# Optimization experiments

Measured on AMD Instinct MI355X. Metric: run time of the kernel, lower is better.

Reference implementation:

```python
import jax, jax.numpy as jnp
import numpy as np

N = 1000000   # total nodes
F = 32        # node feature dim
E = 8         # edge feature dim
K = 16        # kernels per degree
COUNTS = [200000, 300000, 300000, 200000]  # focal nodes per degree 1..4
EPS = 1e-8


def _cos_mat(a, b):
    # a: [n, f], b: [k, f] -> cosine sim [n, k]
    num = a @ b.T
    den = jnp.linalg.norm(a, axis=-1)[:, None] * jnp.linalg.norm(b, axis=-1)[None, :]
    return num / jnp.maximum(den, EPS)


def _cos_pairs(a, b):
    # a: [n, d, f], b: [k, d, f] -> mean over d of per-slot cosine sim -> [n, k]
    num = jnp.einsum('ndf,kdf->nkd', a, b)
    den = jnp.linalg.norm(a, axis=-1)[:, None, :] * jnp.linalg.norm(b, axis=-1)[None, :, :]
    return jnp.mean(num / jnp.maximum(den, EPS), axis=-1)


def _deg_score(x, sel, nei, nei_p, nei_e, Wc, Wn, Wp, We, d):
    nd = sel.shape[0]
    x_focal = x[sel]                     # [nd, F] degree-grouped gather
    x_nei = x[nei].reshape(nd, d, F)     # [nd, d, F]
    sc = (_cos_mat(x_focal, Wc) + _cos_pairs(x_nei, Wn)
          + _cos_pairs(nei_p, Wp) + _cos_pairs(nei_e, We)) * 0.25
    return sc                            # [nd, K]


def setup_inputs() -> dict:
    key = jax.random.key(0)
    ks = iter(jax.random.split(key, 64))
    perm = jax.random.permutation(next(ks), N)  # degree buckets partition all nodes
    inp = {"x": jax.random.normal(next(ks), (N, F), jnp.float32)}
    off = 0
    for d in range(1, 5):
        nd = COUNTS[d - 1]
        inp[f"sel{d}"] = perm[off:off + nd]
        off += nd
        inp[f"nei{d}"] = jax.random.randint(next(ks), (nd * d,), 0, N)
        inp[f"nei_p{d}"] = jax.random.normal(next(ks), (nd, d, 3), jnp.float32)
        inp[f"nei_e{d}"] = jax.random.uniform(next(ks), (nd, d, E), jnp.float32)
        inp[f"Wc{d}"] = jax.random.normal(next(ks), (K, F), jnp.float32)
        inp[f"Wn{d}"] = jax.random.normal(next(ks), (K, d, F), jnp.float32)
        inp[f"Wp{d}"] = jax.random.normal(next(ks), (K, d, 3), jnp.float32)
        inp[f"We{d}"] = jax.random.normal(next(ks), (K, d, E), jnp.float32)
    return inp


def reference(x,
              sel1, nei1, nei_p1, nei_e1, Wc1, Wn1, Wp1, We1,
              sel2, nei2, nei_p2, nei_e2, Wc2, Wn2, Wp2, We2,
              sel3, nei3, nei_p3, nei_e3, Wc3, Wn3, Wp3, We3,
              sel4, nei4, nei_p4, nei_e4, Wc4, Wn4, Wp4, We4):
    groups = [
        (sel1, nei1, nei_p1, nei_e1, Wc1, Wn1, Wp1, We1),
        (sel2, nei2, nei_p2, nei_e2, Wc2, Wn2, Wp2, We2),
        (sel3, nei3, nei_p3, nei_e3, Wc3, Wn3, Wp3, We3),
        (sel4, nei4, nei_p4, nei_e4, Wc4, Wn4, Wp4, We4),
    ]
    # equivalent to: fill [sum_K, N] block matrix grouped by degree, reorder
    # columns by argsort of concatenated selected indices, then transpose.
    out = jnp.zeros((N, 4 * K), x.dtype)
    for i, (sel, nei, npos, ne, wc, wn, wp, we) in enumerate(groups):
        sc = _deg_score(x, sel, nei, npos, ne, wc, wn, wp, we, i + 1)
        out = out.at[sel, i * K:(i + 1) * K].set(sc)
    return out
```

## Files before the change

kernel.cpp:

```cpp
#include <hip/hip_runtime.h>
#include <stdint.h>

typedef _Float16 half8 __attribute__((ext_vector_type(8)));
typedef float floatx4 __attribute__((ext_vector_type(4)));
typedef float fvec4 __attribute__((ext_vector_type(4)));

struct WPtrs { const float *wc, *wn, *wp, *we; };

struct PrepArgs {
  const float* x; _Float16* xhat; int N; int nb_norm;
  WPtrs w[4]; _Float16* psi;
};

__global__ __launch_bounds__(256) void k_prep(PrepArgs a) {
  int bid = blockIdx.x, tid = threadIdx.x;

  if (bid < a.nb_norm) {
    int row = bid * 64 + (tid >> 2);
    int q   = tid & 3;
    if (row >= a.N) return;
    const fvec4* xr = reinterpret_cast<const fvec4*>(a.x + (size_t)row * 32 + q * 8);
    fvec4 va = xr[0], vb = xr[1];
    float ss = va[0] * va[0] + va[1] * va[1] + va[2] * va[2] + va[3] * va[3] +
               vb[0] * vb[0] + vb[1] * vb[1] + vb[2] * vb[2] + vb[3] * vb[3];
    ss += __shfl_xor(ss, 1);
    ss += __shfl_xor(ss, 2);
    float rn = ss > 0.f ? rsqrtf(ss) : 0.f;
    half8 h;
    h[0] = (_Float16)(va[0] * rn); h[1] = (_Float16)(va[1] * rn);
    h[2] = (_Float16)(va[2] * rn); h[3] = (_Float16)(va[3] * rn);
    h[4] = (_Float16)(vb[0] * rn); h[5] = (_Float16)(vb[1] * rn);
    h[6] = (_Float16)(vb[2] * rn); h[7] = (_Float16)(vb[3] * rn);
    *reinterpret_cast<half8*>(a.xhat + (size_t)row * 32 + q * 8) = h;
    return;
  }

  int g = bid - a.nb_norm;
  int d = g + 1;
  int KD = 32 * (1 + d);
  _Float16* pg = a.psi + (size_t)g * (16 * 160);

  int k     = tid & 15;
  int piece = tid >> 4;
  if (piece > d) return;
  const float* src;
  float scale;
  if (piece == 0) { src = a.w[g].wc + k * 32;                           scale = 0.25f; }
  else            { src = a.w[g].wn + (size_t)(k * d + piece - 1) * 32; scale = 0.25f / d; }
  float ss = 0.f;
  for (int j = 0; j < 32; ++j) ss += src[j] * src[j];
  float n  = sqrtf(ss);
  float sc = n > 0.f ? scale / n : 0.f;
  _Float16* dst = pg + k * KD + 32 * piece;
  for (int j = 0; j < 32; ++j) dst[j] = (_Float16)(src[j] * sc);
}

struct MainArgs {
  const _Float16* xhat;
  const _Float16* psi;
  const int* sel[4];
  const int* nei[4];
  const float* p[4];
  const float* e[4];
  WPtrs w[4];
  float* out;
  int nd[4];
  int blkOff[5];
};

template <int D, int NCH>
__device__ inline void main_one(const MainArgs& a, int g, int blk) {
  constexpr int NF = 1 + D;
  constexpr int KD = 32 * NF;
  constexpr int NM = (D + 1) / 2;

  const _Float16* xhat = a.xhat;
  const _Float16* psi  = a.psi + (size_t)g * (16 * 160);
  const int* sel = a.sel[g];
  const int* nei = a.nei[g];
  const float* __restrict__ pptr = a.p[g];
  const float* __restrict__ eptr = a.e[g];
  int nd = a.nd[g];

  int wave    = threadIdx.x >> 6;
  int lane    = threadIdx.x & 63;
  int nchunks = (nd + 15) >> 4;
  int chunk0  = (blk * 4 + wave) * NCH;
  if (chunk0 >= nchunks) return;
  int r = lane & 15;
  int c = lane >> 4;

  half8 bx[NF];
  {
    const _Float16* pb = psi + (size_t)r * KD + c * 8;
#pragma unroll
    for (int t = 0; t < NF; ++t)
      bx[t] = *reinterpret_cast<const half8*>(pb + 32 * t);
  }
  half8 bpe[NM];
#pragma unroll
  for (int m = 0; m < NM; ++m) {
    int s = 2 * m + (c >> 1);
    if (s < D) {
      const float* sp = a.w[g].wp + ((size_t)r * D + s) * 3;
      float a0 = sp[0], a1 = sp[1], a2 = sp[2];
      float n1 = sqrtf(a0 * a0 + a1 * a1 + a2 * a2);
      float s1 = n1 > 0.f ? 0.25f / (D * n1) : 0.f;
      const float* se = a.w[g].we + ((size_t)r * D + s) * 8;
      float b0 = se[0], b1 = se[1], b2 = se[2], b3 = se[3];
      float b4 = se[4], b5 = se[5], b6 = se[6], b7 = se[7];
      float n2 = sqrtf(b0 * b0 + b1 * b1 + b2 * b2 + b3 * b3 +
                       b4 * b4 + b5 * b5 + b6 * b6 + b7 * b7);
      float s2 = n2 > 0.f ? 0.25f / (D * n2) : 0.f;
      half8 h;
      if ((c & 1) == 0) {
        h[0] = (_Float16)(a0 * s1); h[1] = (_Float16)(a1 * s1);
        h[2] = (_Float16)(a2 * s1); h[3] = (_Float16)0.f;
        h[4] = (_Float16)(b0 * s2); h[5] = (_Float16)(b1 * s2);
        h[6] = (_Float16)(b2 * s2); h[7] = (_Float16)(b3 * s2);
      } else {
        h[0] = (_Float16)(b4 * s2); h[1] = (_Float16)(b5 * s2);
        h[2] = (_Float16)(b6 * s2); h[3] = (_Float16)(b7 * s2);
        h[4] = (_Float16)0.f; h[5] = (_Float16)0.f;
        h[6] = (_Float16)0.f; h[7] = (_Float16)0.f;
      }
      bpe[m] = h;
    } else {
      bpe[m] = half8{};
    }
  }

  int riA[NCH];
  int sidx[NCH];
  int gidx[NCH][D];
#pragma unroll
  for (int u = 0; u < NCH; ++u) {
    int chunk = chunk0 + u;
    int ri = (chunk < nchunks) ? (chunk * 16 + r) : 0;
    if (ri > nd - 1) ri = nd - 1;
    riA[u]  = ri;
    sidx[u] = sel[ri];
  }
#pragma unroll
  for (int u = 0; u < NCH; ++u)
#pragma unroll
    for (int s = 0; s < D; ++s)
      gidx[u][s] = nei[(size_t)riA[u] * D + s];

  half8 af[NCH][NF];
#pragma unroll
  for (int u = 0; u < NCH; ++u) {
    af[u][0] = *reinterpret_cast<const half8*>(xhat + (size_t)sidx[u] * 32 + c * 8);
#pragma unroll
    for (int s = 0; s < D; ++s)
      af[u][1 + s] = *reinterpret_cast<const half8*>(xhat + (size_t)gidx[u][s] * 32 + c * 8);
  }

  half8 ap[NCH][NM];
#pragma unroll
  for (int u = 0; u < NCH; ++u) {
#pragma unroll
    for (int m = 0; m < NM; ++m) {
      int s = 2 * m + (c >> 1);
      if (s < D) {
        const float* pp = pptr + ((size_t)riA[u] * D + s) * 3;
        float a0 = pp[0], a1 = pp[1], a2 = pp[2];
        float n1 = sqrtf(a0 * a0 + a1 * a1 + a2 * a2);
        float r1 = n1 > 0.f ? 1.f / n1 : 0.f;
        const fvec4* ee = reinterpret_cast<const fvec4*>(eptr + ((size_t)riA[u] * D + s) * 8);
        fvec4 e0 = ee[0], e1 = ee[1];
        float n2 = sqrtf(e0[0] * e0[0] + e0[1] * e0[1] + e0[2] * e0[2] + e0[3] * e0[3] +
                         e1[0] * e1[0] + e1[1] * e1[1] + e1[2] * e1[2] + e1[3] * e1[3]);
        float r2 = n2 > 0.f ? 1.f / n2 : 0.f;
        half8 h;
        if ((c & 1) == 0) {
          h[0] = (_Float16)(a0 * r1);   h[1] = (_Float16)(a1 * r1);
          h[2] = (_Float16)(a2 * r1);   h[3] = (_Float16)0.f;
          h[4] = (_Float16)(e0[0] * r2); h[5] = (_Float16)(e0[1] * r2);
          h[6] = (_Float16)(e0[2] * r2); h[7] = (_Float16)(e0[3] * r2);
        } else {
          h[0] = (_Float16)(e1[0] * r2); h[1] = (_Float16)(e1[1] * r2);
          h[2] = (_Float16)(e1[2] * r2); h[3] = (_Float16)(e1[3] * r2);
          h[4] = (_Float16)0.f; h[5] = (_Float16)0.f;
          h[6] = (_Float16)0.f; h[7] = (_Float16)0.f;
        }
        ap[u][m] = h;
      } else {
        ap[u][m] = half8{};
      }
    }
  }

  floatx4 acc[NCH];
#pragma unroll
  for (int u = 0; u < NCH; ++u) {
    acc[u] = floatx4{0.f, 0.f, 0.f, 0.f};
#pragma unroll
    for (int m = 0; m < NM; ++m)
      acc[u] = __builtin_amdgcn_mfma_f32_16x16x32_f16(ap[u][m], bpe[m], acc[u], 0, 0, 0);
#pragma unroll
    for (int t = 0; t < NF; ++t)
      acc[u] = __builtin_amdgcn_mfma_f32_16x16x32_f16(af[u][t], bx[t], acc[u], 0, 0, 0);
  }

#pragma unroll
  for (int u = 0; u < NCH; ++u) {
    int chunk = chunk0 + u;
    if (chunk >= nchunks) break;
    int i0 = chunk << 4;
#pragma unroll
    for (int j = 0; j < 4; ++j) {
      int n  = i0 + c * 4 + j;
      int so = __shfl(sidx[u], c * 4 + j);
      if (n < nd) {
        float* orow = a.out + (size_t)so * 64 + r;
#pragma unroll
        for (int q = 0; q < 4; ++q)
          orow[q * 16] = (q == D - 1) ? acc[u][j] : 0.f;
      }
    }
  }
}

__global__ __launch_bounds__(256) void k_main(MainArgs a) {
  int bid = blockIdx.x;
  if (bid < a.blkOff[1])      main_one<1, 6>(a, 0, bid);
  else if (bid < a.blkOff[2]) main_one<2, 5>(a, 1, bid - a.blkOff[1]);
  else if (bid < a.blkOff[3]) main_one<3, 4>(a, 2, bid - a.blkOff[2]);
  else                        main_one<4, 3>(a, 3, bid - a.blkOff[3]);
}

extern "C" void kernel_launch(void* const* d_in, const int* in_sizes, int n_in,
                              void* d_out, int out_size, void* d_ws, size_t ws_size,
                              hipStream_t stream) {
  const float* x = (const float*)d_in[0];
  int N = in_sizes[0] / 32;

  PrepArgs pa;
  MainArgs ma;
  pa.x = x; pa.N = N;
  int nd[4];
  for (int g = 0; g < 4; ++g) {
    int b = 1 + g * 8;
    ma.sel[g]  = (const int*)d_in[b + 0];
    ma.nei[g]  = (const int*)d_in[b + 1];
    ma.p[g]    = (const float*)d_in[b + 2];
    ma.e[g]    = (const float*)d_in[b + 3];
    pa.w[g].wc = (const float*)d_in[b + 4];
    pa.w[g].wn = (const float*)d_in[b + 5];
    pa.w[g].wp = (const float*)d_in[b + 6];
    pa.w[g].we = (const float*)d_in[b + 7];
    ma.w[g]    = pa.w[g];
    nd[g] = in_sizes[b];
    ma.nd[g] = nd[g];
  }
  ma.out = (float*)d_out;

  char* ws = (char*)d_ws;
  auto align256 = [](size_t o) { return (o + 255) & ~(size_t)255; };
  _Float16* xhat = (_Float16*)ws;
  size_t off = align256((size_t)N * 32 * 2);
  _Float16* psi = (_Float16*)(ws + off);
  pa.xhat = xhat;
  pa.psi  = psi;
  ma.xhat = xhat;
  ma.psi  = psi;

  pa.nb_norm = (N + 63) / 64;
  int prep_blocks = pa.nb_norm + 4;

  const int NCHg[4] = {6, 5, 4, 3};
  ma.blkOff[0] = 0;
  for (int g = 0; g < 4; ++g) {
    int ch = (nd[g] + 15) / 16;
    int perBlk = 4 * NCHg[g];
    ma.blkOff[g + 1] = ma.blkOff[g] + (ch + perBlk - 1) / perBlk;
  }

  k_prep<<<prep_blocks, 256, 0, stream>>>(pa);
  k_main<<<ma.blkOff[4], 256, 0, stream>>>(ma);
}
```

Before: 206.6 us.

## Stage normalized position/edge features in LDS with coalesced per-node loads

The position and edge features are no longer loaded redundantly per MFMA lane with scattered 3-float reads. Each thread now reads one node's contiguous p/e rows with vector loads, normalizes them, and writes fp16 A-tiles into shared memory, followed by a barrier before the MFMAs. sqrt+divide is replaced by rsqrt, and the degree-3 chunks per wave drop from 4 to 3 to fit the LDS budget. This costs LDS space, which may lower occupancy, adds a block-wide sync, and the degree-3 change launches more blocks.

```diff
diff --git a/kernel.cpp b/kernel.cpp
--- a/kernel.cpp
+++ b/kernel.cpp
@@ -4,6 +4,7 @@
 typedef _Float16 half8 __attribute__((ext_vector_type(8)));
 typedef float floatx4 __attribute__((ext_vector_type(4)));
 typedef float fvec4 __attribute__((ext_vector_type(4)));
+typedef float fvec2 __attribute__((ext_vector_type(2)));
 
 struct WPtrs { const float *wc, *wn, *wp, *we; };
 
@@ -49,8 +50,7 @@
   else            { src = a.w[g].wn + (size_t)(k * d + piece - 1) * 32; scale = 0.25f / d; }
   float ss = 0.f;
   for (int j = 0; j < 32; ++j) ss += src[j] * src[j];
-  float n  = sqrtf(ss);
-  float sc = n > 0.f ? scale / n : 0.f;
+  float sc = ss > 0.f ? scale * rsqrtf(ss) : 0.f;
   _Float16* dst = pg + k * KD + 32 * piece;
   for (int j = 0; j < 32; ++j) dst[j] = (_Float16)(src[j] * sc);
 }
@@ -69,10 +69,15 @@
 };
 
 template <int D, int NCH>
-__device__ inline void main_one(const MainArgs& a, int g, int blk) {
-  constexpr int NF = 1 + D;
-  constexpr int KD = 32 * NF;
-  constexpr int NM = (D + 1) / 2;
+__device__ inline void main_one(const MainArgs& a, int g, int blk,
+                                _Float16* lds) {
+  constexpr int NF  = 1 + D;
+  constexpr int KD  = 32 * NF;
+  constexpr int K16 = 16 * D;
+  constexpr int K32 = ((D + 1) / 2) * 32;
+  constexpr int NM  = K32 / 32;
+  constexpr int RS  = K32 + 8;
+  constexpr int NN  = 64 * NCH;
 
   const _Float16* xhat = a.xhat;
   const _Float16* psi  = a.psi + (size_t)g * (16 * 160);
@@ -82,13 +87,65 @@
   const float* __restrict__ eptr = a.e[g];
   int nd = a.nd[g];
 
-  int wave    = threadIdx.x >> 6;
-  int lane    = threadIdx.x & 63;
+  int tid  = threadIdx.x;
+  int wave = tid >> 6, lane = tid & 63;
+  int r = lane & 15, c = lane >> 4;
   int nchunks = (nd + 15) >> 4;
-  int chunk0  = (blk * 4 + wave) * NCH;
-  if (chunk0 >= nchunks) return;
-  int r = lane & 15;
-  int c = lane >> 4;
+  size_t base = (size_t)blk * NN;
+
+  for (int l = tid; l < NN; l += 256) {
+    size_t node = base + l;
+    size_t nc = node < (size_t)nd ? node : (size_t)(nd - 1);
+    _Float16* arow = lds + (size_t)l * RS;
+    float pf[3 * D];
+    if constexpr (D == 4) {
+      const fvec4* pv = reinterpret_cast<const fvec4*>(pptr + nc * 12);
+#pragma unroll
+      for (int t = 0; t < 3; ++t) {
+        fvec4 v = pv[t];
+        pf[t * 4 + 0] = v[0]; pf[t * 4 + 1] = v[1];
+        pf[t * 4 + 2] = v[2]; pf[t * 4 + 3] = v[3];
+      }
+    } else if constexpr (D == 2) {
+      const fvec2* pv = reinterpret_cast<const fvec2*>(pptr + nc * 6);
+#pragma unroll
+      for (int t = 0; t < 3; ++t) {
+        fvec2 v = pv[t];
+        pf[t * 2 + 0] = v[0]; pf[t * 2 + 1] = v[1];
+      }
+    } else {
+      const float* pp = pptr + nc * 3 * D;
+#pragma unroll
+      for (int t = 0; t < 3 * D; ++t) pf[t] = pp[t];
+    }
+#pragma unroll
+    for (int s = 0; s < D; ++s) {
+      float a0 = pf[s * 3 + 0], a1 = pf[s * 3 + 1], a2 = pf[s * 3 + 2];
+      float s1 = a0 * a0 + a1 * a1 + a2 * a2;
+      float r1 = s1 > 0.f ? rsqrtf(s1) : 0.f;
+      const fvec4* ee = reinterpret_cast<const fvec4*>(eptr + (nc * D + s) * 8);
+      fvec4 e0 = ee[0], e1 = ee[1];
+      float s2 = e0[0] * e0[0] + e0[1] * e0[1] + e0[2] * e0[2] + e0[3] * e0[3] +
+                 e1[0] * e1[0] + e1[1] * e1[1] + e1[2] * e1[2] + e1[3] * e1[3];
+      float r2 = s2 > 0.f ? rsqrtf(s2) : 0.f;
+      half8 h0, h1;
+      h0[0] = (_Float16)(a0 * r1); h0[1] = (_Float16)(a1 * r1);
+      h0[2] = (_Float16)(a2 * r1); h0[3] = (_Float16)0.f;
+      h0[4] = (_Float16)(e0[0] * r2); h0[5] = (_Float16)(e0[1] * r2);
+      h0[6] = (_Float16)(e0[2] * r2); h0[7] = (_Float16)(e0[3] * r2);
+      h1[0] = (_Float16)(e1[0] * r2); h1[1] = (_Float16)(e1[1] * r2);
+      h1[2] = (_Float16)(e1[2] * r2); h1[3] = (_Float16)(e1[3] * r2);
+      h1[4] = (_Float16)0.f; h1[5] = (_Float16)0.f;
+      h1[6] = (_Float16)0.f; h1[7] = (_Float16)0.f;
+      *reinterpret_cast<half8*>(arow + s * 16)     = h0;
+      *reinterpret_cast<half8*>(arow + s * 16 + 8) = h1;
+    }
+    if (K32 > K16) {
+      half8 z = {};
+      *reinterpret_cast<half8*>(arow + K16)     = z;
+      *reinterpret_cast<half8*>(arow + K16 + 8) = z;
+    }
+  }
 
   half8 bx[NF];
   {
@@ -104,14 +161,14 @@
     if (s < D) {
       const float* sp = a.w[g].wp + ((size_t)r * D + s) * 3;
       float a0 = sp[0], a1 = sp[1], a2 = sp[2];
-      float n1 = sqrtf(a0 * a0 + a1 * a1 + a2 * a2);
-      float s1 = n1 > 0.f ? 0.25f / (D * n1) : 0.f;
+      float q1 = a0 * a0 + a1 * a1 + a2 * a2;
+      float s1 = q1 > 0.f ? 0.25f / D * rsqrtf(q1) : 0.f;
       const float* se = a.w[g].we + ((size_t)r * D + s) * 8;
       float b0 = se[0], b1 = se[1], b2 = se[2], b3 = se[3];
       float b4 = se[4], b5 = se[5], b6 = se[6], b7 = se[7];
-      float n2 = sqrtf(b0 * b0 + b1 * b1 + b2 * b2 + b3 * b3 +
-                       b4 * b4 + b5 * b5 + b6 * b6 + b7 * b7);
-      float s2 = n2 > 0.f ? 0.25f / (D * n2) : 0.f;
+      float q2 = b0 * b0 + b1 * b1 + b2 * b2 + b3 * b3 +
+                 b4 * b4 + b5 * b5 + b6 * b6 + b7 * b7;
+      float s2 = q2 > 0.f ? 0.25f / D * rsqrtf(q2) : 0.f;
       half8 h;
       if ((c & 1) == 0) {
         h[0] = (_Float16)(a0 * s1); h[1] = (_Float16)(a1 * s1);
@@ -130,23 +187,17 @@
     }
   }
 
-  int riA[NCH];
   int sidx[NCH];
   int gidx[NCH][D];
 #pragma unroll
   for (int u = 0; u < NCH; ++u) {
-    int chunk = chunk0 + u;
-    int ri = (chunk < nchunks) ? (chunk * 16 + r) : 0;
+    int ri = (int)base + (wave * NCH + u) * 16 + r;
     if (ri > nd - 1) ri = nd - 1;
-    riA[u]  = ri;
     sidx[u] = sel[ri];
-  }
-#pragma unroll
-  for (int u = 0; u < NCH; ++u)
 #pragma unroll
     for (int s = 0; s < D; ++s)
-      gidx[u][s] = nei[(size_t)riA[u] * D + s];
-
+      gidx[u][s] = nei[(size_t)ri * D + s];
+  }
   half8 af[NCH][NF];
 #pragma unroll
   for (int u = 0; u < NCH; ++u) {
@@ -156,78 +207,46 @@
       af[u][1 + s] = *reinterpret_cast<const half8*>(xhat + (size_t)gidx[u][s] * 32 + c * 8);
   }
 
-  half8 ap[NCH][NM];
+  __syncthreads();
+
 #pragma unroll
   for (int u = 0; u < NCH; ++u) {
+    floatx4 acc = {0.f, 0.f, 0.f, 0.f};
+    const _Float16* arow = lds + (size_t)((wave * NCH + u) * 16 + r) * RS + c * 8;
 #pragma unroll
     for (int m = 0; m < NM; ++m) {
-      int s = 2 * m + (c >> 1);
-      if (s < D) {
-        const float* pp = pptr + ((size_t)riA[u] * D + s) * 3;
-        float a0 = pp[0], a1 = pp[1], a2 = pp[2];
-        float n1 = sqrtf(a0 * a0 + a1 * a1 + a2 * a2);
-        float r1 = n1 > 0.f ? 1.f / n1 : 0.f;
-        const fvec4* ee = reinterpret_cast<const fvec4*>(eptr + ((size_t)riA[u] * D + s) * 8);
-        fvec4 e0 = ee[0], e1 = ee[1];
-        float n2 = sqrtf(e0[0] * e0[0] + e0[1] * e0[1] + e0[2] * e0[2] + e0[3] * e0[3] +
-                         e1[0] * e1[0] + e1[1] * e1[1] + e1[2] * e1[2] + e1[3] * e1[3]);
-        float r2 = n2 > 0.f ? 1.f / n2 : 0.f;
-        half8 h;
-        if ((c & 1) == 0) {
-          h[0] = (_Float16)(a0 * r1);   h[1] = (_Float16)(a1 * r1);
-          h[2] = (_Float16)(a2 * r1);   h[3] = (_Float16)0.f;
-          h[4] = (_Float16)(e0[0] * r2); h[5] = (_Float16)(e0[1] * r2);
-          h[6] = (_Float16)(e0[2] * r2); h[7] = (_Float16)(e0[3] * r2);
-        } else {
-          h[0] = (_Float16)(e1[0] * r2); h[1] = (_Float16)(e1[1] * r2);
-          h[2] = (_Float16)(e1[2] * r2); h[3] = (_Float16)(e1[3] * r2);
-          h[4] = (_Float16)0.f; h[5] = (_Float16)0.f;
-          h[6] = (_Float16)0.f; h[7] = (_Float16)0.f;
+      half8 ap = *reinterpret_cast<const half8*>(arow + m * 32);
+      acc = __builtin_amdgcn_mfma_f32_16x16x32_f16(ap, bpe[m], acc, 0, 0, 0);
+    }
+#pragma unroll
+    for (int t = 0; t < NF; ++t)
+      acc = __builtin_amdgcn_mfma_f32_16x16x32_f16(af[u][t], bx[t], acc, 0, 0, 0);
+
+    int chunk = blk * (4 * NCH) + wave * NCH + u;
+    if (chunk < nchunks) {
+      int i0 = chunk << 4;
+#pragma unroll
+      for (int j = 0; j < 4; ++j) {
+        int n  = i0 + c * 4 + j;
+        int so = __shfl(sidx[u], c * 4 + j);
+        if (n < nd) {
+          float* orow = a.out + (size_t)so * 64 + r;
+#pragma unroll
+          for (int q = 0; q < 4; ++q)
+            orow[q * 16] = (q == D - 1) ? acc[j] : 0.f;
         }
-        ap[u][m] = h;
-      } else {
-        ap[u][m] = half8{};
       }
     }
   }
-
-  floatx4 acc[NCH];
-#pragma unroll
-  for (int u = 0; u < NCH; ++u) {
-    acc[u] = floatx4{0.f, 0.f, 0.f, 0.f};
-#pragma unroll
-    for (int m = 0; m < NM; ++m)
-      acc[u] = __builtin_amdgcn_mfma_f32_16x16x32_f16(ap[u][m], bpe[m], acc[u], 0, 0, 0);
-#pragma unroll
-    for (int t = 0; t < NF; ++t)
-      acc[u] = __builtin_amdgcn_mfma_f32_16x16x32_f16(af[u][t], bx[t], acc[u], 0, 0, 0);
-  }
-
-#pragma unroll
-  for (int u = 0; u < NCH; ++u) {
-    int chunk = chunk0 + u;
-    if (chunk >= nchunks) break;
-    int i0 = chunk << 4;
-#pragma unroll
-    for (int j = 0; j < 4; ++j) {
-      int n  = i0 + c * 4 + j;
-      int so = __shfl(sidx[u], c * 4 + j);
-      if (n < nd) {
-        float* orow = a.out + (size_t)so * 64 + r;
-#pragma unroll
-        for (int q = 0; q < 4; ++q)
-          orow[q * 16] = (q == D - 1) ? acc[u][j] : 0.f;
-      }
-    }
-  }
 }
 
 __global__ __launch_bounds__(256) void k_main(MainArgs a) {
+  __shared__ __align__(16) _Float16 lds[15360];
   int bid = blockIdx.x;
-  if (bid < a.blkOff[1])      main_one<1, 6>(a, 0, bid);
-  else if (bid < a.blkOff[2]) main_one<2, 5>(a, 1, bid - a.blkOff[1]);
-  else if (bid < a.blkOff[3]) main_one<3, 4>(a, 2, bid - a.blkOff[2]);
-  else                        main_one<4, 3>(a, 3, bid - a.blkOff[3]);
+  if (bid < a.blkOff[1])      main_one<1, 6>(a, 0, bid,               lds);
+  else if (bid < a.blkOff[2]) main_one<2, 5>(a, 1, bid - a.blkOff[1], lds);
+  else if (bid < a.blkOff[3]) main_one<3, 3>(a, 2, bid - a.blkOff[2], lds);
+  else                        main_one<4, 3>(a, 3, bid - a.blkOff[3], lds);
 }
 
 extern "C" void kernel_launch(void* const* d_in, const int* in_sizes, int n_in,
@@ -269,7 +288,7 @@
   pa.nb_norm = (N + 63) / 64;
   int prep_blocks = pa.nb_norm + 4;
 
-  const int NCHg[4] = {6, 5, 4, 3};
+  const int NCHg[4] = {6, 5, 3, 3};
   ma.blkOff[0] = 0;
   for (int g = 0; g < 4; ++g) {
     int ch = (nd[g] + 15) / 16;
```

Measured after the change: 170.9 us. -17.3%, faster.
